# Optimization experiments

Hardware: AMD Instinct MI355X
Metric: run time of the kernel (lower is better)

The kernel has to match this reference:

```python
import jax, jax.numpy as jnp
import numpy as np

N_HEAD = 8
HEAD_DIM = 64
DIM = 512
INNER = N_HEAD * HEAD_DIM
ATT_THRESHOLD = 1e-4
SCALE = HEAD_DIM ** -0.5


def setup_inputs() -> dict:
    key = jax.random.key(0)
    ks = jax.random.split(key, 7)
    b, n, dn = 2, 2048, 2048
    fr = jax.random.normal(ks[0], (b, n, DIM), dtype=jnp.float32)
    dt = jax.random.normal(ks[1], (b, dn, DIM), dtype=jnp.float32)
    s = DIM ** -0.5
    Wq = jax.random.normal(ks[2], (DIM, INNER), dtype=jnp.float32) * s
    Wk = jax.random.normal(ks[3], (DIM, INNER), dtype=jnp.float32) * s
    Wv = jax.random.normal(ks[4], (DIM, INNER), dtype=jnp.float32) * s
    Wo = jax.random.normal(ks[5], (INNER, DIM), dtype=jnp.float32) * (INNER ** -0.5)
    bo = jax.random.normal(ks[6], (DIM,), dtype=jnp.float32) * 0.01
    return {"fr": fr, "dt": dt, "Wq": Wq, "Wk": Wk, "Wv": Wv, "Wo": Wo, "bo": bo}


def reference(fr, dt, Wq, Wk, Wv, Wo, bo):
    b, n, _ = fr.shape
    dn = dt.shape[1]
    # projections -> [b, seq, n_head, head_dim]
    q = (fr @ Wq).reshape(b, n, N_HEAD, HEAD_DIM)
    k = (dt @ Wk).reshape(b, dn, N_HEAD, HEAD_DIM)
    v = (dt @ Wv).reshape(b, dn, N_HEAD, HEAD_DIM)
    # full attention matrix [b, h, n, dn]
    scores = jnp.einsum('bihd,bjhd->bhij', q, k) * SCALE
    attn = jax.nn.softmax(scores, axis=-1)
    # torch .clip(t) with one positional arg clamps the MIN: max(attn, t)
    attn = jnp.maximum(attn, ATT_THRESHOLD) - ATT_THRESHOLD
    attn = attn / jnp.sum(attn, axis=-1, keepdims=True)
    out = jnp.einsum('bhij,bjhd->bihd', attn, v).reshape(b, n, INNER)
    return out @ Wo + bo
```

## Files before the change

### kernel.cpp

```cpp
#include <hip/hip_runtime.h>
#include <hip/hip_bf16.h>

#define BB 2
#define SEQ 2048
#define NHEAD 8
#define HD 64
#define ATT_T 1e-4f
#define QSCALE 0.18033688011112042f

typedef short s16x8 __attribute__((ext_vector_type(8)));
typedef float f32x16 __attribute__((ext_vector_type(16)));

#define MFMA32(a, b, c) __builtin_amdgcn_mfma_f32_32x32x16_bf16((a), (b), (c), 0, 0, 0)
#define EXP2(x) __builtin_amdgcn_exp2f(x)
#define SB0() __builtin_amdgcn_sched_barrier(0)
#define WAITVM0() __builtin_amdgcn_s_waitcnt(0x0F70)
#define WAITVM4() __builtin_amdgcn_s_waitcnt(0x0F74)
#define WAITVM8() __builtin_amdgcn_s_waitcnt(0x0F78)

__device__ __forceinline__ unsigned short bfr(float x) {
  __hip_bfloat16 h = __float2bfloat16(x);
  return __builtin_bit_cast(unsigned short, h);
}
__device__ __forceinline__ unsigned int packbf(float a, float b) {
  return (unsigned int)bfr(a) | ((unsigned int)bfr(b) << 16);
}
__device__ __forceinline__ void async16(const void* g, void* l) {
  __builtin_amdgcn_global_load_lds(
      (const __attribute__((address_space(1))) unsigned int*)g,
      (__attribute__((address_space(3))) unsigned int*)l, 16, 0, 0);
}

__global__ __launch_bounds__(256) void prep(const float* __restrict__ fr,
                                            const float* __restrict__ dt,
                                            const float* __restrict__ w0,
                                            const float* __restrict__ w1,
                                            const float* __restrict__ w2,
                                            const float* __restrict__ w3,
                                            unsigned short* __restrict__ frB,
                                            unsigned short* __restrict__ dtB,
                                            unsigned short* __restrict__ o0,
                                            unsigned short* __restrict__ o1,
                                            unsigned short* __restrict__ o2,
                                            unsigned short* __restrict__ o3) {
  __shared__ float tle[64][65];
  const int bid = blockIdx.x;
  if (bid < 4096) {
    const float* x = bid < 2048 ? fr : dt;
    unsigned short* y = bid < 2048 ? frB : dtB;
    size_t i = ((size_t)(bid & 2047) * 256 + threadIdx.x) * 4;
    float4 v = *(const float4*)(x + i);
    uint2 p;
    p.x = packbf(v.x, v.y);
    p.y = packbf(v.z, v.w);
    *(uint2*)(y + i) = p;
    return;
  }
  const int idx = bid - 4096;
  const int z = idx >> 6;
  const float* W = z == 0 ? w0 : z == 1 ? w1 : z == 2 ? w2 : w3;
  unsigned short* WT = z == 0 ? o0 : z == 1 ? o1 : z == 2 ? o2 : o3;
  const int r0 = ((idx >> 3) & 7) * 64, c0 = (idx & 7) * 64;
  const int tr = threadIdx.x >> 4;
  const int tc = threadIdx.x & 15;
  #pragma unroll
  for (int i = 0; i < 4; i++) {
    int r = tr + i * 16;
    float4 v = *(const float4*)(W + (size_t)(r0 + r) * 512 + c0 + tc * 4);
    tle[r][tc * 4 + 0] = v.x;
    tle[r][tc * 4 + 1] = v.y;
    tle[r][tc * 4 + 2] = v.z;
    tle[r][tc * 4 + 3] = v.w;
  }
  __syncthreads();
  #pragma unroll
  for (int i = 0; i < 4; i++) {
    int c = tr + i * 16;
    int rr = tc * 4;
    uint2 p;
    p.x = packbf(tle[rr + 0][c], tle[rr + 1][c]);
    p.y = packbf(tle[rr + 2][c], tle[rr + 3][c]);
    *(uint2*)(WT + (size_t)(c0 + c) * 512 + r0 + rr) = p;
  }
}

__device__ __forceinline__ void gemm_core_bk64(const unsigned short* __restrict__ A,
                                               const unsigned short* __restrict__ BT,
                                               unsigned short* smem, int m0, int n0,
                                               int w, int lane, f32x16 (&acc)[2]) {
  unsigned short* Asm = smem;
  unsigned short* Bsm = smem + 8192;
  const int l31 = lane & 31, lh = lane >> 5;

  auto stage = [&](int kt, int buf) {
    const int k0 = kt * 64;
    #pragma unroll
    for (int i = 0; i < 2; i++) {
      int r = w * 2 + i, g = r >> 2, ks = r & 3;
      async16(A + (size_t)(m0 + g * 32 + l31) * 512 + k0 + ks * 16 + lh * 8,
              Asm + buf * 4096 + r * 512);
    }
    #pragma unroll
    for (int i = 0; i < 4; i++) {
      int r = w * 4 + i, gn = r >> 2, ks = r & 3;
      async16(BT + (size_t)(n0 + gn * 32 + l31) * 512 + k0 + ks * 16 + lh * 8,
              Bsm + buf * 8192 + r * 512);
    }
  };

  stage(0, 0);
  for (int kt = 0; kt < 8; ++kt) {
    __syncthreads();
    if (kt + 1 < 8) stage(kt + 1, (kt + 1) & 1);
    const int buf = kt & 1;
    const unsigned short* as = Asm + buf * 4096 + (w & 1) * 2048;
    const unsigned short* bs = Bsm + buf * 8192 + (w >> 1) * 4096;
    #pragma unroll
    for (int ks = 0; ks < 4; ++ks) {
      s16x8 af = *(const s16x8*)(as + ks * 512 + lane * 8);
      s16x8 b0 = *(const s16x8*)(bs + ks * 512 + lane * 8);
      s16x8 b1 = *(const s16x8*)(bs + 2048 + ks * 512 + lane * 8);
      acc[0] = MFMA32(af, b0, acc[0]);
      acc[1] = MFMA32(af, b1, acc[1]);
    }
  }
}

__global__ __launch_bounds__(256) void gemm_qkv(const unsigned short* __restrict__ frB,
                                                const unsigned short* __restrict__ dtB,
                                                const unsigned short* __restrict__ WqT,
                                                const unsigned short* __restrict__ WkT,
                                                const unsigned short* __restrict__ WvT,
                                                unsigned short* __restrict__ Qp,
                                                unsigned short* __restrict__ Kp,
                                                unsigned short* __restrict__ VTp) {
  __shared__ __align__(16) unsigned short smem[24576];
  const int tid = threadIdx.x, lane = tid & 63, w = tid >> 6;
  const int l31 = lane & 31, lh = lane >> 5;
  const int m0 = blockIdx.y * 64, n0 = blockIdx.x * 128;
  const int z = blockIdx.z;
  const unsigned short* A = z == 0 ? frB : dtB;
  const unsigned short* BT = z == 0 ? WqT : (z == 1 ? WkT : WvT);
  unsigned short* OP = z == 0 ? Qp : (z == 1 ? Kp : VTp);
  const float scale = z == 0 ? QSCALE : 1.0f;

  f32x16 acc[2];
  #pragma unroll
  for (int j = 0; j < 2; j++)
    #pragma unroll
    for (int r = 0; r < 16; r++) acc[j][r] = 0.f;

  gemm_core_bk64(A, BT, smem, m0, n0, w, lane, acc);

  const int wm = (w & 1) * 32, wn = (w >> 1) * 64;
  const int bb = m0 >> 11, s0 = m0 & 2047;
  __syncthreads();
  if (z <= 1) {
    #pragma unroll
    for (int j = 0; j < 2; j++)
      #pragma unroll
      for (int r = 0; r < 16; r++) {
        int mm = wm + (r & 3) + 8 * (r >> 2) + 4 * lh;
        int nn = wn + j * 32 + l31;
        smem[mm * 136 + nn] = bfr(acc[j][r] * scale);
      }
    __syncthreads();
    #pragma unroll
    for (int it = 0; it < 4; ++it) {
      int c = tid + it * 256;
      int mm = c >> 4, seg = c & 15;
      uint4 vdat = *(const uint4*)(smem + mm * 136 + seg * 8);
      int n = n0 + seg * 8, h = n >> 6, d = n & 63;
      *(uint4*)(OP + ((size_t)((bb * NHEAD + h) * SEQ + s0 + mm)) * HD + d) = vdat;
    }
  } else {
    #pragma unroll
    for (int j = 0; j < 2; j++)
      #pragma unroll
      for (int r = 0; r < 16; r += 2) {
        int mm = wm + (r & 3) + 8 * (r >> 2) + 4 * lh;
        int nn = wn + j * 32 + l31;
        *(unsigned int*)(smem + nn * 72 + mm) = packbf(acc[j][r], acc[j][r + 1]);
      }
    __syncthreads();
    #pragma unroll
    for (int it = 0; it < 4; ++it) {
      int c = tid + it * 256;
      int nn = c >> 3, seg = c & 7;
      uint4 vdat = *(const uint4*)(smem + nn * 72 + seg * 8);
      int n = n0 + nn, h = n >> 6, d = n & 63;
      *(uint4*)(OP + ((size_t)((bb * NHEAD + h) * HD + d)) * SEQ + s0 + seg * 8) = vdat;
    }
  }
}

__global__ __launch_bounds__(256) void gemm_out(const unsigned short* __restrict__ A,
                                                const unsigned short* __restrict__ BT,
                                                const float* __restrict__ bias,
                                                float* __restrict__ O) {
  __shared__ __align__(16) unsigned short smem[24576];
  const int tid = threadIdx.x, lane = tid & 63, w = tid >> 6;
  const int l31 = lane & 31, lh = lane >> 5;
  const int m0 = blockIdx.y * 64, n0 = blockIdx.x * 128;

  f32x16 acc[2];
  #pragma unroll
  for (int j = 0; j < 2; j++)
    #pragma unroll
    for (int r = 0; r < 16; r++) acc[j][r] = 0.f;

  gemm_core_bk64(A, BT, smem, m0, n0, w, lane, acc);

  const int wm = (w & 1) * 32, wn = (w >> 1) * 64;
  #pragma unroll
  for (int j = 0; j < 2; j++) {
    float bv = bias[n0 + wn + j * 32 + l31];
    #pragma unroll
    for (int r = 0; r < 16; r++) {
      int mm = wm + (r & 3) + 8 * (r >> 2) + 4 * lh;
      O[(size_t)(m0 + mm) * 512 + n0 + wn + j * 32 + l31] = acc[j][r] + bv;
    }
  }
}

__global__ __launch_bounds__(256, 2) void attn_mfma(const unsigned short* __restrict__ Q,
                                                    const unsigned short* __restrict__ K,
                                                    const unsigned short* __restrict__ VT,
                                                    unsigned short* __restrict__ O) {
  __shared__ __align__(16) unsigned short arena[4][8192];
  __shared__ float larr[4][64];
  __shared__ float warr[4][64];

  const int tid = threadIdx.x;
  const int lane = tid & 63;
  const int w = tid >> 6;
  const int l31 = lane & 31, lh = lane >> 5;

  const int bid = blockIdx.x;
  const int g = bid & 7, j = bid >> 3;
  const int bh = g * 2 + (j >> 5);
  const int qt = j & 31;

  const unsigned short* Qh = Q + (size_t)bh * SEQ * HD;
  const unsigned short* Kh = K + (size_t)bh * SEQ * HD;
  const unsigned short* VTh = VT + (size_t)bh * HD * SEQ;

  s16x8 qf[2][4];
  #pragma unroll
  for (int q2 = 0; q2 < 2; q2++)
    #pragma unroll
    for (int t = 0; t < 4; t++)
      qf[q2][t] = *(const s16x8*)(Qh + (size_t)(qt * 64 + q2 * 32 + l31) * HD + 16 * t + 8 * lh);

  unsigned short* kbuf = &arena[w][0];
  unsigned short* vbuf = &arena[w][4096];
  const int kbase = w * 512;

  auto stageK = [&](int c, int slot) {
    const unsigned short* base = Kh + (size_t)(kbase + c * 32 + l31) * HD + lh * 8;
    #pragma unroll
    for (int tt = 0; tt < 4; tt++)
      async16(base + tt * 16, kbuf + slot * 2048 + tt * 512);
  };
  auto stageV = [&](int c, int slot) {
    #pragma unroll
    for (int dh = 0; dh < 2; dh++)
      #pragma unroll
      for (int kc = 0; kc < 2; kc++)
        async16(VTh + (size_t)(dh * 32 + l31) * SEQ + kbase + c * 32 + kc * 16 + lh * 8,
                vbuf + slot * 2048 + (dh * 2 + kc) * 512);
  };

  float lsum[2] = {0.f, 0.f};
  stageK(0, 0);
  for (int c = 0; c < 16; ++c) {
    const int slot = c & 1;
    if (c + 1 < 16) {
      stageK(c + 1, slot ^ 1);
      SB0();
      WAITVM4();
      SB0();
    } else {
      SB0();
      WAITVM0();
      SB0();
    }
    s16x8 kf[4];
    #pragma unroll
    for (int tt = 0; tt < 4; tt++)
      kf[tt] = *(const s16x8*)(kbuf + slot * 2048 + tt * 512 + lane * 8);
    #pragma unroll
    for (int q2 = 0; q2 < 2; q2++) {
      f32x16 sc;
      #pragma unroll
      for (int r = 0; r < 16; r++) sc[r] = 0.f;
      #pragma unroll
      for (int tt = 0; tt < 4; tt++) sc = MFMA32(kf[tt], qf[q2][tt], sc);
      float s0 = 0.f, s1 = 0.f, s2 = 0.f, s3 = 0.f;
      #pragma unroll
      for (int r = 0; r < 4; r++) {
        s0 += EXP2(sc[r]);
        s1 += EXP2(sc[4 + r]);
        s2 += EXP2(sc[8 + r]);
        s3 += EXP2(sc[12 + r]);
      }
      lsum[q2] += (s0 + s1) + (s2 + s3);
    }
  }
  #pragma unroll
  for (int q2 = 0; q2 < 2; q2++) lsum[q2] += __shfl_xor(lsum[q2], 32);
  if (lh == 0) { larr[w][l31] = lsum[0]; larr[w][32 + l31] = lsum[1]; }
  __syncthreads();
  float tl[2];
  #pragma unroll
  for (int q2 = 0; q2 < 2; q2++)
    tl[q2] = ATT_T * (larr[0][q2 * 32 + l31] + larr[1][q2 * 32 + l31] +
                      larr[2][q2 * 32 + l31] + larr[3][q2 * 32 + l31]);

  f32x16 acc[2][2];
  #pragma unroll
  for (int q2 = 0; q2 < 2; q2++)
    #pragma unroll
    for (int dh = 0; dh < 2; dh++)
      #pragma unroll
      for (int r = 0; r < 16; r++) acc[q2][dh][r] = 0.f;
  float wacc[2] = {0.f, 0.f};

  stageK(0, 0);
  stageV(0, 0);
  for (int c = 0; c < 16; ++c) {
    const int slot = c & 1;
    if (c + 1 < 16) {
      stageK(c + 1, slot ^ 1);
      stageV(c + 1, slot ^ 1);
      SB0();
      WAITVM8();
      SB0();
    } else {
      SB0();
      WAITVM0();
      SB0();
    }
    s16x8 kf[4], vf[2][2];
    #pragma unroll
    for (int tt = 0; tt < 4; tt++)
      kf[tt] = *(const s16x8*)(kbuf + slot * 2048 + tt * 512 + lane * 8);
    #pragma unroll
    for (int dh = 0; dh < 2; dh++)
      #pragma unroll
      for (int kc = 0; kc < 2; kc++)
        vf[dh][kc] = *(const s16x8*)(vbuf + slot * 2048 + (dh * 2 + kc) * 512 + lane * 8);
    s16x8 pf[2][2];
    #pragma unroll
    for (int q2 = 0; q2 < 2; q2++) {
      f32x16 sc;
      #pragma unroll
      for (int r = 0; r < 16; r++) sc[r] = 0.f;
      #pragma unroll
      for (int tt = 0; tt < 4; tt++) sc = MFMA32(kf[tt], qf[q2][tt], sc);
      uint2 quads[4];
      #pragma unroll
      for (int gq = 0; gq < 4; gq++) {
        float u0 = fmaxf(EXP2(sc[4 * gq + 0]) - tl[q2], 0.f);
        float u1 = fmaxf(EXP2(sc[4 * gq + 1]) - tl[q2], 0.f);
        float u2 = fmaxf(EXP2(sc[4 * gq + 2]) - tl[q2], 0.f);
        float u3 = fmaxf(EXP2(sc[4 * gq + 3]) - tl[q2], 0.f);
        wacc[q2] += (u0 + u1) + (u2 + u3);
        quads[gq].x = packbf(u0, u1);
        quads[gq].y = packbf(u2, u3);
      }
      #pragma unroll
      for (int tp = 0; tp < 2; tp++) {
        uint2 ea, eb;
        ea.x = (unsigned)__shfl_xor((int)quads[2 * tp].x, 32);
        ea.y = (unsigned)__shfl_xor((int)quads[2 * tp].y, 32);
        eb.x = (unsigned)__shfl_xor((int)quads[2 * tp + 1].x, 32);
        eb.y = (unsigned)__shfl_xor((int)quads[2 * tp + 1].y, 32);
        uint4 fr;
        if (lh == 0) { fr.x = quads[2 * tp].x; fr.y = quads[2 * tp].y; fr.z = ea.x; fr.w = ea.y; }
        else         { fr.x = eb.x; fr.y = eb.y; fr.z = quads[2 * tp + 1].x; fr.w = quads[2 * tp + 1].y; }
        pf[q2][tp] = __builtin_bit_cast(s16x8, fr);
      }
    }
    #pragma unroll
    for (int q2 = 0; q2 < 2; q2++)
      #pragma unroll
      for (int dh = 0; dh < 2; dh++) {
        acc[q2][dh] = MFMA32(pf[q2][0], vf[dh][0], acc[q2][dh]);
        acc[q2][dh] = MFMA32(pf[q2][1], vf[dh][1], acc[q2][dh]);
      }
  }

  #pragma unroll
  for (int q2 = 0; q2 < 2; q2++) wacc[q2] += __shfl_xor(wacc[q2], 32);
  if (lh == 0) { warr[w][l31] = wacc[0]; warr[w][32 + l31] = wacc[1]; }
  __syncthreads();

  float* plane0 = (float*)&arena[0][0];
  float* plane1 = (float*)&arena[2][0];

  if (w >= 2) {
    float* pl = (w == 2) ? plane0 : plane1;
    #pragma unroll
    for (int q2 = 0; q2 < 2; q2++)
      #pragma unroll
      for (int dh = 0; dh < 2; dh++)
        #pragma unroll
        for (int r = 0; r < 16; r++) {
          int ql = q2 * 32 + (r & 3) + 8 * (r >> 2) + 4 * lh;
          pl[ql * 64 + dh * 32 + l31] = acc[q2][dh][r];
        }
  }
  __syncthreads();
  if (w < 2) {
    float* pl = (w == 0) ? plane0 : plane1;
    #pragma unroll
    for (int q2 = 0; q2 < 2; q2++)
      #pragma unroll
      for (int dh = 0; dh < 2; dh++)
        #pragma unroll
        for (int r = 0; r < 16; r++) {
          int ql = q2 * 32 + (r & 3) + 8 * (r >> 2) + 4 * lh;
          acc[q2][dh][r] += pl[ql * 64 + dh * 32 + l31];
        }
  }
  __syncthreads();
  if (w == 1) {
    #pragma unroll
    for (int q2 = 0; q2 < 2; q2++)
      #pragma unroll
      for (int dh = 0; dh < 2; dh++)
        #pragma unroll
        for (int r = 0; r < 16; r++) {
          int ql = q2 * 32 + (r & 3) + 8 * (r >> 2) + 4 * lh;
          plane0[ql * 64 + dh * 32 + l31] = acc[q2][dh][r];
        }
  }
  __syncthreads();
  unsigned short* otile = &arena[2][0];
  if (w == 0) {
    #pragma unroll
    for (int q2 = 0; q2 < 2; q2++)
      #pragma unroll
      for (int dh = 0; dh < 2; dh++)
        #pragma unroll
        for (int r = 0; r < 16; r++) {
          int ql = q2 * 32 + (r & 3) + 8 * (r >> 2) + 4 * lh;
          float wt = warr[0][ql] + warr[1][ql] + warr[2][ql] + warr[3][ql];
          float v = (acc[q2][dh][r] + plane0[ql * 64 + dh * 32 + l31]) / wt;
          otile[ql * 64 + dh * 32 + l31] = bfr(v);
        }
  }
  __syncthreads();
  const int b = bh >> 3, h = bh & 7;
  #pragma unroll
  for (int it = 0; it < 2; ++it) {
    int c2 = tid + it * 256;
    int mm = c2 >> 3, seg = c2 & 7;
    uint4 vdat = *(const uint4*)(otile + mm * 64 + seg * 8);
    *(uint4*)(O + ((size_t)(b * SEQ + qt * 64 + mm)) * 512 + h * HD + seg * 8) = vdat;
  }
}

extern "C" void kernel_launch(void* const* d_in, const int* in_sizes, int n_in,
                              void* d_out, int out_size, void* d_ws, size_t ws_size,
                              hipStream_t stream) {
  const float* fr = (const float*)d_in[0];
  const float* dt = (const float*)d_in[1];
  const float* Wq = (const float*)d_in[2];
  const float* Wk = (const float*)d_in[3];
  const float* Wv = (const float*)d_in[4];
  const float* Wo = (const float*)d_in[5];
  const float* bo = (const float*)d_in[6];
  float* out = (float*)d_out;

  const size_t planeE = (size_t)BB * SEQ * 512;
  const size_t wE = 512 * 512;
  unsigned short* p = (unsigned short*)d_ws;
  unsigned short* frB = p; p += planeE;
  unsigned short* dtB = p; p += planeE;
  unsigned short* WqT = p; p += wE;
  unsigned short* WkT = p; p += wE;
  unsigned short* WvT = p; p += wE;
  unsigned short* WoT = p; p += wE;
  unsigned short* Qp  = p; p += planeE;
  unsigned short* Kp  = p; p += planeE;
  unsigned short* VTp = p; p += planeE;
  unsigned short* aoB = p; p += planeE;

  prep<<<4352, 256, 0, stream>>>(fr, dt, Wq, Wk, Wv, Wo, frB, dtB, WqT, WkT, WvT, WoT);

  gemm_qkv<<<dim3(4, 64, 3), 256, 0, stream>>>(frB, dtB, WqT, WkT, WvT, Qp, Kp, VTp);

  attn_mfma<<<BB * NHEAD * 32, 256, 0, stream>>>(Qp, Kp, VTp, aoB);

  gemm_out<<<dim3(4, 64), 256, 0, stream>>>(aoB, WoT, bo, out);
}
```

Before: 165.8 us.

## Software-pipeline QK scores so exp/softmax overlaps next chunk's loads and MFMAs

Both attention passes now keep the QK^T score tile for chunk c in registers and do its exp, threshold and PV MFMA work in the next iteration. That work runs after the next K/V async loads are issued and before waiting on them, so exp and VALU work can hide load latency and interleave with MFMAs. The float-to-bf16 packing of probabilities is also replaced by a byte-permute truncation instead of round-to-nearest. The cost is more live registers for the carried score and V fragments, which may hurt occupancy, and slightly different rounding of P.

```diff
diff --git a/kernel.cpp b/kernel.cpp
--- a/kernel.cpp
+++ b/kernel.cpp
@@ -24,6 +24,10 @@
 }
 __device__ __forceinline__ unsigned int packbf(float a, float b) {
   return (unsigned int)bfr(a) | ((unsigned int)bfr(b) << 16);
+}
+__device__ __forceinline__ unsigned int permpack(float a, float b) {
+  return __builtin_amdgcn_perm(__builtin_bit_cast(unsigned int, b),
+                               __builtin_bit_cast(unsigned int, a), 0x07060302u);
 }
 __device__ __forceinline__ void async16(const void* g, void* l) {
   __builtin_amdgcn_global_load_lds(
@@ -272,19 +276,30 @@
   };
 
   float lsum[2] = {0.f, 0.f};
+  f32x16 scp[2];
+
+  auto accum_l = [&]() {
+    #pragma unroll
+    for (int q2 = 0; q2 < 2; q2++) {
+      float s0 = 0.f, s1 = 0.f, s2 = 0.f, s3 = 0.f;
+      #pragma unroll
+      for (int r = 0; r < 4; r++) {
+        s0 += EXP2(scp[q2][r]);
+        s1 += EXP2(scp[q2][4 + r]);
+        s2 += EXP2(scp[q2][8 + r]);
+        s3 += EXP2(scp[q2][12 + r]);
+      }
+      lsum[q2] += (s0 + s1) + (s2 + s3);
+    }
+  };
+
   stageK(0, 0);
   for (int c = 0; c < 16; ++c) {
     const int slot = c & 1;
-    if (c + 1 < 16) {
-      stageK(c + 1, slot ^ 1);
-      SB0();
-      WAITVM4();
-      SB0();
-    } else {
-      SB0();
-      WAITVM0();
-      SB0();
-    }
+    if (c + 1 < 16) stageK(c + 1, slot ^ 1);
+    if (c > 0) accum_l();
+    if (c + 1 < 16) { WAITVM4(); } else { WAITVM0(); }
+    SB0();
     s16x8 kf[4];
     #pragma unroll
     for (int tt = 0; tt < 4; tt++)
@@ -296,17 +311,10 @@
       for (int r = 0; r < 16; r++) sc[r] = 0.f;
       #pragma unroll
       for (int tt = 0; tt < 4; tt++) sc = MFMA32(kf[tt], qf[q2][tt], sc);
-      float s0 = 0.f, s1 = 0.f, s2 = 0.f, s3 = 0.f;
-      #pragma unroll
-      for (int r = 0; r < 4; r++) {
-        s0 += EXP2(sc[r]);
-        s1 += EXP2(sc[4 + r]);
-        s2 += EXP2(sc[8 + r]);
-        s3 += EXP2(sc[12 + r]);
-      }
-      lsum[q2] += (s0 + s1) + (s2 + s3);
-    }
-  }
+      scp[q2] = sc;
+    }
+  }
+  accum_l();
   #pragma unroll
   for (int q2 = 0; q2 < 2; q2++) lsum[q2] += __shfl_xor(lsum[q2], 32);
   if (lh == 0) { larr[w][l31] = lsum[0]; larr[w][32 + l31] = lsum[1]; }
@@ -325,49 +333,22 @@
       #pragma unroll
       for (int r = 0; r < 16; r++) acc[q2][dh][r] = 0.f;
   float wacc[2] = {0.f, 0.f};
-
-  stageK(0, 0);
-  stageV(0, 0);
-  for (int c = 0; c < 16; ++c) {
-    const int slot = c & 1;
-    if (c + 1 < 16) {
-      stageK(c + 1, slot ^ 1);
-      stageV(c + 1, slot ^ 1);
-      SB0();
-      WAITVM8();
-      SB0();
-    } else {
-      SB0();
-      WAITVM0();
-      SB0();
-    }
-    s16x8 kf[4], vf[2][2];
-    #pragma unroll
-    for (int tt = 0; tt < 4; tt++)
-      kf[tt] = *(const s16x8*)(kbuf + slot * 2048 + tt * 512 + lane * 8);
-    #pragma unroll
-    for (int dh = 0; dh < 2; dh++)
-      #pragma unroll
-      for (int kc = 0; kc < 2; kc++)
-        vf[dh][kc] = *(const s16x8*)(vbuf + slot * 2048 + (dh * 2 + kc) * 512 + lane * 8);
+  s16x8 vfp[2][2];
+
+  auto softmax_pv = [&]() {
     s16x8 pf[2][2];
     #pragma unroll
     for (int q2 = 0; q2 < 2; q2++) {
-      f32x16 sc;
-      #pragma unroll
-      for (int r = 0; r < 16; r++) sc[r] = 0.f;
-      #pragma unroll
-      for (int tt = 0; tt < 4; tt++) sc = MFMA32(kf[tt], qf[q2][tt], sc);
       uint2 quads[4];
       #pragma unroll
       for (int gq = 0; gq < 4; gq++) {
-        float u0 = fmaxf(EXP2(sc[4 * gq + 0]) - tl[q2], 0.f);
-        float u1 = fmaxf(EXP2(sc[4 * gq + 1]) - tl[q2], 0.f);
-        float u2 = fmaxf(EXP2(sc[4 * gq + 2]) - tl[q2], 0.f);
-        float u3 = fmaxf(EXP2(sc[4 * gq + 3]) - tl[q2], 0.f);
+        float u0 = fmaxf(EXP2(scp[q2][4 * gq + 0]) - tl[q2], 0.f);
+        float u1 = fmaxf(EXP2(scp[q2][4 * gq + 1]) - tl[q2], 0.f);
+        float u2 = fmaxf(EXP2(scp[q2][4 * gq + 2]) - tl[q2], 0.f);
+        float u3 = fmaxf(EXP2(scp[q2][4 * gq + 3]) - tl[q2], 0.f);
         wacc[q2] += (u0 + u1) + (u2 + u3);
-        quads[gq].x = packbf(u0, u1);
-        quads[gq].y = packbf(u2, u3);
+        quads[gq].x = permpack(u0, u1);
+        quads[gq].y = permpack(u2, u3);
       }
       #pragma unroll
       for (int tp = 0; tp < 2; tp++) {
@@ -386,10 +367,39 @@
     for (int q2 = 0; q2 < 2; q2++)
       #pragma unroll
       for (int dh = 0; dh < 2; dh++) {
-        acc[q2][dh] = MFMA32(pf[q2][0], vf[dh][0], acc[q2][dh]);
-        acc[q2][dh] = MFMA32(pf[q2][1], vf[dh][1], acc[q2][dh]);
+        acc[q2][dh] = MFMA32(pf[q2][0], vfp[dh][0], acc[q2][dh]);
+        acc[q2][dh] = MFMA32(pf[q2][1], vfp[dh][1], acc[q2][dh]);
       }
-  }
+  };
+
+  stageK(0, 0);
+  stageV(0, 0);
+  for (int c = 0; c < 16; ++c) {
+    const int slot = c & 1;
+    if (c + 1 < 16) { stageK(c + 1, slot ^ 1); stageV(c + 1, slot ^ 1); }
+    if (c > 0) softmax_pv();
+    if (c + 1 < 16) { WAITVM8(); } else { WAITVM0(); }
+    SB0();
+    s16x8 kf[4];
+    #pragma unroll
+    for (int tt = 0; tt < 4; tt++)
+      kf[tt] = *(const s16x8*)(kbuf + slot * 2048 + tt * 512 + lane * 8);
+    #pragma unroll
+    for (int dh = 0; dh < 2; dh++)
+      #pragma unroll
+      for (int kc = 0; kc < 2; kc++)
+        vfp[dh][kc] = *(const s16x8*)(vbuf + slot * 2048 + (dh * 2 + kc) * 512 + lane * 8);
+    #pragma unroll
+    for (int q2 = 0; q2 < 2; q2++) {
+      f32x16 sc;
+      #pragma unroll
+      for (int r = 0; r < 16; r++) sc[r] = 0.f;
+      #pragma unroll
+      for (int tt = 0; tt < 4; tt++) sc = MFMA32(kf[tt], qf[q2][tt], sc);
+      scp[q2] = sc;
+    }
+  }
+  softmax_pv();
 
   #pragma unroll
   for (int q2 = 0; q2 < 2; q2++) wacc[q2] += __shfl_xor(wacc[q2], 32);
```

Measured after the change: 166.1 us. No clear change (+0.2%).
